# Kernel tuning notes

Measured on AMD Instinct MI355X. Metric: run time of the kernel, lower is better.

## Reference

```python
import jax, jax.numpy as jnp
import numpy as np

DIM = 768
HEADS = 12
HD = DIM // HEADS
B = 8
N = 1025  # 1 cls token + 32x32 patch grid
NUM_CLS = 1
ROPE_BASE = 100.0


def setup_inputs() -> dict:
    key = jax.random.key(0)
    ks = jax.random.split(key, 4)
    x = jax.random.normal(ks[0], (B, N, DIM), jnp.float32)
    xpos = jax.random.randint(ks[1], (B, N, 2), 0, 32)  # int 2D grid coords
    mask_for_attention = jnp.ones((B, N, N), dtype=bool)
    w_qkv = jax.random.normal(ks[2], (3 * DIM, DIM), jnp.float32) / np.sqrt(DIM)
    w_proj = jax.random.normal(ks[3], (DIM, DIM), jnp.float32) / np.sqrt(DIM)
    b_proj = jnp.zeros((DIM,), jnp.float32)
    return {"num_cls": NUM_CLS, "x": x, "xpos": xpos,
            "mask_for_attention": mask_for_attention,
            "w_qkv": w_qkv, "w_proj": w_proj, "b_proj": b_proj}


def _rope1d(t, pos):
    # t: [B,H,N,d], pos: [B,N] float. croco-style: cos/sin table of size d = cat(f,f),
    # rotate_half(x) = cat(-x2, x1).
    d = t.shape[-1]
    inv = 1.0 / (ROPE_BASE ** (jnp.arange(0, d, 2, dtype=jnp.float32) / d))  # [d/2]
    ang = pos[..., None] * inv  # [B,N,d/2]
    cos = jnp.concatenate([jnp.cos(ang), jnp.cos(ang)], -1)[:, None]  # [B,1,N,d]
    sin = jnp.concatenate([jnp.sin(ang), jnp.sin(ang)], -1)[:, None]
    t1, t2 = jnp.split(t, 2, -1)
    rot = jnp.concatenate([-t2, t1], -1)
    return t * cos + rot * sin


def _rope2d(t, pos):
    # first half of head_dim rotated by y coord, second half by x coord
    d = t.shape[-1] // 2
    py = pos[..., 0].astype(t.dtype)
    px = pos[..., 1].astype(t.dtype)
    return jnp.concatenate([_rope1d(t[..., :d], py), _rope1d(t[..., d:], px)], -1)


def reference(num_cls, x, xpos, mask_for_attention, w_qkv, w_proj, b_proj):
    Bb, Nn, C = x.shape
    H, hd = HEADS, C // HEADS
    scale = hd ** -0.5
    # qkv projection -> [B,H,3,N,hd] (mirrors torch .transpose(1,3))
    qkv = (x @ w_qkv.T).reshape(Bb, Nn, 3, H, hd).transpose(0, 3, 2, 1, 4)
    q, k, v = qkv[:, :, 0], qkv[:, :, 1], qkv[:, :, 2]
    # RoPE on non-cls tokens only
    q_nc = _rope2d(q[:, :, num_cls:], xpos[:, num_cls:])
    k_nc = _rope2d(k[:, :, num_cls:], xpos[:, num_cls:])
    # block-structured sim matrix
    sim_rope = jnp.einsum('bhqd,bhkd->bhqk', q_nc, k_nc)            # [B,H,N-c,N-c]
    sim_qcls_k = jnp.einsum('bhqd,bhkd->bhqk', q[:, :, :num_cls], k[:, :, num_cls:])  # [B,H,c,N-c]
    sim_q = jnp.einsum('bhqd,bhkd->bhqk', q, k[:, :, :num_cls])      # [B,H,N,c]
    sim = jnp.concatenate([sim_q,
                           jnp.concatenate([sim_qcls_k, sim_rope], axis=-2)],
                          axis=-1)  # [B,H,N,N]
    sim = sim * scale
    sim = jnp.where(mask_for_attention[:, None], sim, -jnp.inf)
    attn = jax.nn.softmax(sim, axis=-1)
    out = jnp.einsum('bhqk,bhkd->bhqd', attn, v)
    out = out.transpose(0, 2, 1, 3).reshape(Bb, Nn, C)
    return out @ w_proj.T + b_proj
```

## Files before the change

### kernel.cpp

```cpp
#include <hip/hip_runtime.h>

#define Bb 8
#define Nn 1025
#define Hh 12
#define HD 64
#define DIMC 768
#define QKVC 2304
#define MROWS (Bb * Nn)
#define MPADA 8320
#define NPAD 1152
#define K1 0.180336880111f
#define PADCNT 127.0f

typedef _Float16 f16x8 __attribute__((ext_vector_type(8)));
typedef _Float16 f16x4 __attribute__((ext_vector_type(4)));
typedef float f32x4 __attribute__((ext_vector_type(4)));

typedef const __attribute__((address_space(1))) void gv_t;
typedef __attribute__((address_space(3))) void lv_t;

__global__ void cvt3_kernel(const float* __restrict__ s0, _Float16* __restrict__ d0, int n0,
                            const float* __restrict__ s1, _Float16* __restrict__ d1, int n1,
                            const float* __restrict__ s2, _Float16* __restrict__ d2, int n2) {
    int i = blockIdx.x * 256 + threadIdx.x;
    const float* s; _Float16* d; int j;
    if (i < n0)           { s = s0; d = d0; j = i; }
    else if (i < n0 + n1) { s = s1; d = d1; j = i - n0; }
    else if (i < n0 + n1 + n2) { s = s2; d = d2; j = i - n0 - n1; }
    else return;
    float4 v = ((const float4*)s)[j];
    f16x4 h;
    h.x = (_Float16)v.x; h.y = (_Float16)v.y; h.z = (_Float16)v.z; h.w = (_Float16)v.w;
    ((f16x4*)d)[j] = h;
}

template <int MODE>
__global__ void __launch_bounds__(256) gemm_kernel(
    const _Float16* __restrict__ A, const _Float16* __restrict__ W,
    int M, int Ncols, int K,
    _Float16* __restrict__ outh, const float* __restrict__ bias, float* __restrict__ outf)
{
    __shared__ _Float16 As[128 * 32];
    __shared__ _Float16 Ws[128 * 32];
    const int tid = threadIdx.x;
    const int wid = tid >> 6, lane = tid & 63;
    const int quad = lane >> 4, l16 = lane & 15;
    const int bm = blockIdx.x * 128, bn = blockIdx.y * 128;
    const int wm = (wid >> 1) * 64, wn = (wid & 1) * 64;

    f32x4 acc[4][4] = {};

    for (int kk = 0; kk < K; kk += 32) {
#pragma unroll
        for (int c = 0; c < 2; ++c) {
            int s = c * 256 + tid;
            int row = s >> 2, gr = s & 3;
            const _Float16* ga = A + (size_t)(bm + row) * K + kk + gr * 8;
            const _Float16* gw = W + (size_t)(bn + row) * K + kk + gr * 8;
            _Float16* la = As + (size_t)(c * 256 + wid * 64) * 8;
            _Float16* lw = Ws + (size_t)(c * 256 + wid * 64) * 8;
            __builtin_amdgcn_global_load_lds((gv_t*)ga, (lv_t*)la, 16, 0, 0);
            __builtin_amdgcn_global_load_lds((gv_t*)gw, (lv_t*)lw, 16, 0, 0);
        }
        __syncthreads();

        f16x8 af[4], bf[4];
#pragma unroll
        for (int t = 0; t < 4; ++t) {
            af[t] = *(const f16x8*)(As + (size_t)(wm + t * 16 + l16) * 32 + quad * 8);
            bf[t] = *(const f16x8*)(Ws + (size_t)(wn + t * 16 + l16) * 32 + quad * 8);
        }
#pragma unroll
        for (int tm = 0; tm < 4; ++tm)
#pragma unroll
            for (int tn = 0; tn < 4; ++tn)
                acc[tm][tn] = __builtin_amdgcn_mfma_f32_16x16x32_f16(af[tm], bf[tn], acc[tm][tn], 0, 0, 0);
        __syncthreads();
    }

#pragma unroll
    for (int tm = 0; tm < 4; ++tm) {
#pragma unroll
        for (int r = 0; r < 4; ++r) {
            int row = bm + wm + tm * 16 + quad * 4 + r;
            if (row >= M) continue;
#pragma unroll
            for (int tn = 0; tn < 4; ++tn) {
                int col = bn + wn + tn * 16 + l16;
                float val = acc[tm][tn][r];
                if (MODE == 0) {
                    outh[(size_t)row * Ncols + col] = (_Float16)val;
                } else {
                    outf[(size_t)row * Ncols + col] = val + bias[col];
                }
            }
        }
    }
}

__global__ void __launch_bounds__(256) vtrans_kernel(
    const _Float16* __restrict__ qkv, _Float16* __restrict__ vt)
{
    __shared__ _Float16 Ts[64][72];
    const int nt = blockIdx.x;
    const int bh = blockIdx.y;
    const int b = bh / Hh, h = bh - b * Hh;
    const int n0 = nt * 64;
    const int tid = threadIdx.x;
    const _Float16* vsrc = qkv + (size_t)b * Nn * QKVC + 2 * DIMC + h * HD;
#pragma unroll
    for (int i = 0; i < 2; ++i) {
        int t = tid + i * 256;
        int r = t >> 3, cg = t & 7;
        int gn = n0 + r;
        f16x8 v8 = {};
        if (gn < Nn) v8 = *(const f16x8*)(vsrc + (size_t)gn * QKVC + cg * 8);
        *(f16x8*)&Ts[r][cg * 8] = v8;
    }
    __syncthreads();
#pragma unroll
    for (int i = 0; i < 2; ++i) {
        int t = tid + i * 256;
        int d = t >> 3, ng = t & 7;
        f16x8 o;
#pragma unroll
        for (int s = 0; s < 8; ++s) o[s] = Ts[ng * 8 + s][d];
        *(f16x8*)(vt + ((size_t)bh * HD + d) * NPAD + n0 + ng * 8) = o;
    }
}

__global__ void __launch_bounds__(256) rope_kernel(
    _Float16* __restrict__ qkv, const int* __restrict__ xpos,
    float* __restrict__ col0, float* __restrict__ row0)
{
    int gw = blockIdx.x * 4 + (threadIdx.x >> 6);
    int lane = threadIdx.x & 63;
    if (gw >= Bb * Hh * Nn) return;
    int n = gw % Nn;
    int bh = gw / Nn;
    int b = bh / Hh, h = bh - b * Hh;

    _Float16* qp = qkv + ((size_t)b * Nn + n) * QKVC + h * HD;
    _Float16* kp = qp + DIMC;
    const _Float16* qp0 = qkv + (size_t)b * Nn * QKVC + h * HD;
    const _Float16* kp0 = qp0 + DIMC;

    float q = (float)qp[lane];
    float k = (float)kp[lane];
    float q0 = (float)qp0[lane];
    float k0 = (float)kp0[lane];

    float dcol = q * k0, drow = q0 * k;
#pragma unroll
    for (int off = 1; off < 64; off <<= 1) {
        dcol += __shfl_xor(dcol, off);
        drow += __shfl_xor(drow, off);
    }
    if (lane == 0) {
        col0[gw] = dcol * K1;
        row0[gw] = drow * K1;
    }

    if (n >= 1) {
        int py = xpos[((size_t)b * Nn + n) * 2 + 0];
        int px = xpos[((size_t)b * Nn + n) * 2 + 1];
        float pos = (lane < 32) ? (float)py : (float)px;
        int j = lane & 15;
        float inv = __expf(-0.28782313662f * (float)j);
        float ang = pos * inv;
        float sv = __sinf(ang), cv = __cosf(ang);
        float qp_ = __shfl_xor(q, 16);
        float kp_ = __shfl_xor(k, 16);
        float sgn = (lane & 16) ? 1.0f : -1.0f;
        qp[lane] = (_Float16)((q * cv + sgn * qp_ * sv) * K1);
        kp[lane] = (_Float16)(k * cv + sgn * kp_ * sv);
    }
}

__global__ void __launch_bounds__(256) flash_kernel(
    const _Float16* __restrict__ qkv, const _Float16* __restrict__ vt,
    const float* __restrict__ col0, const float* __restrict__ row0,
    _Float16* __restrict__ att)
{
    __shared__ _Float16 Ks[128][72];
    __shared__ _Float16 Vt[64][136];
    __shared__ _Float16 Ps[64][136];

    const int qt = blockIdx.x, bh = blockIdx.y;
    const int b = bh / Hh, h = bh - b * Hh;
    const int tid = threadIdx.x, wid = tid >> 6, lane = tid & 63;
    const int quad = lane >> 4, l16 = lane & 15;
    const int q0row = qt * 64;
    const int c0base = bh * Nn;
    const _Float16* qg = qkv + (size_t)b * Nn * QKVC + h * HD;
    const _Float16* kg = qg + DIMC;
    const _Float16* vtg = vt + (size_t)bh * HD * NPAD;

    const int kR = tid >> 3, kC = (tid & 7) * 8;
    const int vD = tid >> 4, vC = (tid & 15) * 8;

#pragma unroll
    for (int i = 0; i < 2; ++i) {
        int t = tid + i * 256;
        int r = t >> 3, cg = t & 7;
        int gr = q0row + r;
        f16x8 v8 = {};
        if (gr < Nn) v8 = *(const f16x8*)(qg + (size_t)gr * QKVC + cg * 8);
        *(f16x8*)&Ks[r][cg * 8] = v8;
    }
    __syncthreads();
    f16x8 aq[2];
#pragma unroll
    for (int ks = 0; ks < 2; ++ks)
        aq[ks] = *(const f16x8*)&Ks[wid * 16 + l16][ks * 32 + quad * 8];
    __syncthreads();

    f32x4 oacc[4] = {};
    float lrow[4] = {0.f, 0.f, 0.f, 0.f};
    const int gibase = q0row + wid * 16 + quad * 4;

    f16x8 kreg[4], vreg[4];
#pragma unroll
    for (int i = 0; i < 4; ++i) {
        int gr = kR + i * 32;
        f16x8 v8 = {};
        if (gr < Nn) v8 = *(const f16x8*)(kg + (size_t)gr * QKVC + kC);
        kreg[i] = v8;
        vreg[i] = *(const f16x8*)(vtg + (size_t)(vD + i * 16) * NPAD + vC);
    }

    for (int c0 = 0; c0 < Nn; c0 += 128) {
#pragma unroll
        for (int i = 0; i < 4; ++i) {
            *(f16x8*)&Ks[kR + i * 32][kC] = kreg[i];
            *(f16x8*)&Vt[vD + i * 16][vC] = vreg[i];
        }
        __syncthreads();

        int cn = c0 + 128;
        if (cn < Nn) {
#pragma unroll
            for (int i = 0; i < 4; ++i) {
                int gr = cn + kR + i * 32;
                f16x8 v8 = {};
                if (gr < Nn) v8 = *(const f16x8*)(kg + (size_t)gr * QKVC + kC);
                kreg[i] = v8;
                vreg[i] = *(const f16x8*)(vtg + (size_t)(vD + i * 16) * NPAD + cn + vC);
            }
        }

        f32x4 sacc[8] = {};
#pragma unroll
        for (int ks = 0; ks < 2; ++ks)
#pragma unroll
            for (int ct = 0; ct < 8; ++ct) {
                f16x8 bk = *(const f16x8*)&Ks[ct * 16 + l16][ks * 32 + quad * 8];
                sacc[ct] = __builtin_amdgcn_mfma_f32_16x16x32_f16(aq[ks], bk, sacc[ct], 0, 0, 0);
            }

        if (c0 == 0 && l16 == 0) {
#pragma unroll
            for (int r = 0; r < 4; ++r) {
                int gi = gibase + r;
                sacc[0][r] = col0[c0base + (gi < Nn ? gi : 0)];
            }
        }
        if (q0row == 0 && wid == 0 && quad == 0) {
#pragma unroll
            for (int ct = 0; ct < 8; ++ct) {
                int gj = c0 + ct * 16 + l16;
                if (gj < Nn) sacc[ct][0] = row0[c0base + gj];
            }
        }

#pragma unroll
        for (int ct = 0; ct < 8; ++ct) {
#pragma unroll
            for (int r = 0; r < 4; ++r) {
                float p = exp2f(sacc[ct][r]);
                lrow[r] += p;
                Ps[wid * 16 + quad * 4 + r][ct * 16 + l16] = (_Float16)p;
            }
        }

#pragma unroll
        for (int ks = 0; ks < 4; ++ks) {
            f16x8 ap = *(const f16x8*)&Ps[wid * 16 + l16][ks * 32 + quad * 8];
#pragma unroll
            for (int ct = 0; ct < 4; ++ct) {
                f16x8 bv = *(const f16x8*)&Vt[ct * 16 + l16][ks * 32 + quad * 8];
                oacc[ct] = __builtin_amdgcn_mfma_f32_16x16x32_f16(ap, bv, oacc[ct], 0, 0, 0);
            }
        }
        __syncthreads();
    }

#pragma unroll
    for (int r = 0; r < 4; ++r) {
        float l = lrow[r];
#pragma unroll
        for (int off = 1; off < 16; off <<= 1) l += __shfl_xor(l, off);
        l -= PADCNT;
        int gi = q0row + wid * 16 + quad * 4 + r;
        if (gi >= Nn) continue;
        float inv_l = 1.0f / l;
#pragma unroll
        for (int ct = 0; ct < 4; ++ct) {
            att[((size_t)b * Nn + gi) * DIMC + h * HD + ct * 16 + l16] =
                (_Float16)(oacc[ct][r] * inv_l);
        }
    }
}

extern "C" void kernel_launch(void* const* d_in, const int* in_sizes, int n_in,
                              void* d_out, int out_size, void* d_ws, size_t ws_size,
                              hipStream_t stream) {
    const float* x      = (const float*)d_in[1];
    const int*   xpos   = (const int*)d_in[2];
    const float* w_qkv  = (const float*)d_in[4];
    const float* w_proj = (const float*)d_in[5];
    const float* b_proj = (const float*)d_in[6];
    float* out = (float*)d_out;

    char* ws = (char*)d_ws;
    size_t off = 0;
    auto alloc = [&](size_t bytes) {
        char* p = ws + off;
        off += (bytes + 255) & ~(size_t)255;
        return p;
    };
    _Float16* xh     = (_Float16*)alloc((size_t)MPADA * DIMC * 2);
    _Float16* qkvh   = (_Float16*)alloc((size_t)MROWS * QKVC * 2);
    _Float16* vt     = (_Float16*)alloc((size_t)Bb * Hh * HD * NPAD * 2);
    _Float16* wqkvh  = (_Float16*)alloc((size_t)3 * DIMC * DIMC * 2);
    _Float16* wprojh = (_Float16*)alloc((size_t)DIMC * DIMC * 2);
    float* col0      = (float*)alloc((size_t)Bb * Hh * Nn * 4);
    float* row0      = (float*)alloc((size_t)Bb * Hh * Nn * 4);
    _Float16* atth   = xh;

    {
        int n0 = (MROWS * DIMC) / 4;
        int n1 = (3 * DIMC * DIMC) / 4;
        int n2 = (DIMC * DIMC) / 4;
        int nt = n0 + n1 + n2;
        cvt3_kernel<<<(nt + 255) / 256, 256, 0, stream>>>(
            x, xh, n0, w_qkv, wqkvh, n1, w_proj, wprojh, n2);
    }

    gemm_kernel<0><<<dim3(MPADA / 128, QKVC / 128), 256, 0, stream>>>(
        xh, wqkvh, MROWS, QKVC, DIMC, qkvh, nullptr, nullptr);

    rope_kernel<<<(Bb * Hh * Nn) / 4, 256, 0, stream>>>(qkvh, xpos, col0, row0);

    vtrans_kernel<<<dim3(NPAD / 64, Bb * Hh), 256, 0, stream>>>(qkvh, vt);

    flash_kernel<<<dim3((Nn + 63) / 64, Bb * Hh), 256, 0, stream>>>(
        qkvh, vt, col0, row0, atth);

    gemm_kernel<1><<<dim3(MPADA / 128, DIMC / 128), 256, 0, stream>>>(
        atth, wprojh, MROWS, DIMC, DIMC, nullptr, b_proj, out);
}
```

Measured before the change: 303.1 us.

## Keep softmax probabilities in registers via transposed MFMA; double K-step in GEMM

The flash kernel now computes S transposed (K as the A operand, Q as B), so each lane holds a query column. The probabilities are packed to fp16 with cvt_pkrtz and rearranged with cross-lane shuffles into the B operand of the PV MFMA, which removes the LDS round trip through the Ps buffer. It also changes the row-sum reduction and makes the output stores vectorized. Separately, the GEMM loads two 32-wide K slices per barrier pair, which halves the synchronisation count at the cost of double the shared memory. The cvt_pkrtz conversion rounds toward zero, a slight precision change.

```diff
diff --git a/kernel.cpp b/kernel.cpp
--- a/kernel.cpp
+++ b/kernel.cpp
@@ -14,7 +14,9 @@
 
 typedef _Float16 f16x8 __attribute__((ext_vector_type(8)));
 typedef _Float16 f16x4 __attribute__((ext_vector_type(4)));
+typedef _Float16 f16x2 __attribute__((ext_vector_type(2)));
 typedef float f32x4 __attribute__((ext_vector_type(4)));
+typedef int i32x4 __attribute__((ext_vector_type(4)));
 
 typedef const __attribute__((address_space(1))) void gv_t;
 typedef __attribute__((address_space(3))) void lv_t;
@@ -40,8 +42,8 @@
     int M, int Ncols, int K,
     _Float16* __restrict__ outh, const float* __restrict__ bias, float* __restrict__ outf)
 {
-    __shared__ _Float16 As[128 * 32];
-    __shared__ _Float16 Ws[128 * 32];
+    __shared__ _Float16 As[2][128 * 32];
+    __shared__ _Float16 Ws[2][128 * 32];
     const int tid = threadIdx.x;
     const int wid = tid >> 6, lane = tid & 63;
     const int quad = lane >> 4, l16 = lane & 15;
@@ -50,31 +52,37 @@
 
     f32x4 acc[4][4] = {};
 
-    for (int kk = 0; kk < K; kk += 32) {
-#pragma unroll
-        for (int c = 0; c < 2; ++c) {
-            int s = c * 256 + tid;
-            int row = s >> 2, gr = s & 3;
-            const _Float16* ga = A + (size_t)(bm + row) * K + kk + gr * 8;
-            const _Float16* gw = W + (size_t)(bn + row) * K + kk + gr * 8;
-            _Float16* la = As + (size_t)(c * 256 + wid * 64) * 8;
-            _Float16* lw = Ws + (size_t)(c * 256 + wid * 64) * 8;
-            __builtin_amdgcn_global_load_lds((gv_t*)ga, (lv_t*)la, 16, 0, 0);
-            __builtin_amdgcn_global_load_lds((gv_t*)gw, (lv_t*)lw, 16, 0, 0);
+    for (int kk = 0; kk < K; kk += 64) {
+#pragma unroll
+        for (int half = 0; half < 2; ++half) {
+#pragma unroll
+            for (int c = 0; c < 2; ++c) {
+                int s = c * 256 + tid;
+                int row = s >> 2, gr = s & 3;
+                const _Float16* ga = A + (size_t)(bm + row) * K + kk + half * 32 + gr * 8;
+                const _Float16* gw = W + (size_t)(bn + row) * K + kk + half * 32 + gr * 8;
+                _Float16* la = As[half] + (size_t)(c * 256 + wid * 64) * 8;
+                _Float16* lw = Ws[half] + (size_t)(c * 256 + wid * 64) * 8;
+                __builtin_amdgcn_global_load_lds((gv_t*)ga, (lv_t*)la, 16, 0, 0);
+                __builtin_amdgcn_global_load_lds((gv_t*)gw, (lv_t*)lw, 16, 0, 0);
+            }
         }
         __syncthreads();
 
-        f16x8 af[4], bf[4];
-#pragma unroll
-        for (int t = 0; t < 4; ++t) {
-            af[t] = *(const f16x8*)(As + (size_t)(wm + t * 16 + l16) * 32 + quad * 8);
-            bf[t] = *(const f16x8*)(Ws + (size_t)(wn + t * 16 + l16) * 32 + quad * 8);
-        }
-#pragma unroll
-        for (int tm = 0; tm < 4; ++tm)
-#pragma unroll
-            for (int tn = 0; tn < 4; ++tn)
-                acc[tm][tn] = __builtin_amdgcn_mfma_f32_16x16x32_f16(af[tm], bf[tn], acc[tm][tn], 0, 0, 0);
+#pragma unroll
+        for (int half = 0; half < 2; ++half) {
+            f16x8 af[4], bf[4];
+#pragma unroll
+            for (int t = 0; t < 4; ++t) {
+                af[t] = *(const f16x8*)(As[half] + (size_t)(wm + t * 16 + l16) * 32 + quad * 8);
+                bf[t] = *(const f16x8*)(Ws[half] + (size_t)(wn + t * 16 + l16) * 32 + quad * 8);
+            }
+#pragma unroll
+            for (int tm = 0; tm < 4; ++tm)
+#pragma unroll
+                for (int tn = 0; tn < 4; ++tn)
+                    acc[tm][tn] = __builtin_amdgcn_mfma_f32_16x16x32_f16(af[tm], bf[tn], acc[tm][tn], 0, 0, 0);
+        }
         __syncthreads();
     }
 
@@ -184,7 +192,6 @@
 {
     __shared__ _Float16 Ks[128][72];
     __shared__ _Float16 Vt[64][136];
-    __shared__ _Float16 Ps[64][136];
 
     const int qt = blockIdx.x, bh = blockIdx.y;
     const int b = bh / Hh, h = bh - b * Hh;
@@ -215,9 +222,13 @@
         aq[ks] = *(const f16x8*)&Ks[wid * 16 + l16][ks * 32 + quad * 8];
     __syncthreads();
 
-    f32x4 oacc[4] = {};
-    float lrow[4] = {0.f, 0.f, 0.f, 0.f};
-    const int gibase = q0row + wid * 16 + quad * 4;
+    f32x4 oaccT[4] = {};
+    float lrow = 0.f;
+    const int gi = q0row + wid * 16 + l16;
+
+    const int src0 = (((2 * quad) & 3) << 4) + l16;
+    const int src1 = (((2 * quad + 1) & 3) << 4) + l16;
+    const bool hi = (quad >= 2);
 
     f16x8 kreg[4], vreg[4];
 #pragma unroll
@@ -254,60 +265,68 @@
         for (int ks = 0; ks < 2; ++ks)
 #pragma unroll
             for (int ct = 0; ct < 8; ++ct) {
-                f16x8 bk = *(const f16x8*)&Ks[ct * 16 + l16][ks * 32 + quad * 8];
-                sacc[ct] = __builtin_amdgcn_mfma_f32_16x16x32_f16(aq[ks], bk, sacc[ct], 0, 0, 0);
-            }
-
-        if (c0 == 0 && l16 == 0) {
-#pragma unroll
-            for (int r = 0; r < 4; ++r) {
-                int gi = gibase + r;
-                sacc[0][r] = col0[c0base + (gi < Nn ? gi : 0)];
-            }
-        }
-        if (q0row == 0 && wid == 0 && quad == 0) {
-#pragma unroll
-            for (int ct = 0; ct < 8; ++ct) {
-                int gj = c0 + ct * 16 + l16;
-                if (gj < Nn) sacc[ct][0] = row0[c0base + gj];
-            }
-        }
-
+                f16x8 ak = *(const f16x8*)&Ks[ct * 16 + l16][ks * 32 + quad * 8];
+                sacc[ct] = __builtin_amdgcn_mfma_f32_16x16x32_f16(ak, aq[ks], sacc[ct], 0, 0, 0);
+            }
+
+        if (c0 == 0 && quad == 0)
+            sacc[0][0] = col0[c0base + (gi < Nn ? gi : 0)];
+        if (q0row == 0 && wid == 0 && l16 == 0) {
+#pragma unroll
+            for (int ct = 0; ct < 8; ++ct)
+#pragma unroll
+                for (int r = 0; r < 4; ++r) {
+                    int gj = c0 + ct * 16 + quad * 4 + r;
+                    if (gj < Nn) sacc[ct][r] = row0[c0base + gj];
+                }
+        }
+
+        int pkl[8], pkh[8];
 #pragma unroll
         for (int ct = 0; ct < 8; ++ct) {
-#pragma unroll
-            for (int r = 0; r < 4; ++r) {
-                float p = exp2f(sacc[ct][r]);
-                lrow[r] += p;
-                Ps[wid * 16 + quad * 4 + r][ct * 16 + l16] = (_Float16)p;
-            }
+            float p0 = exp2f(sacc[ct][0]);
+            float p1 = exp2f(sacc[ct][1]);
+            float p2 = exp2f(sacc[ct][2]);
+            float p3 = exp2f(sacc[ct][3]);
+            lrow += (p0 + p1) + (p2 + p3);
+            pkl[ct] = __builtin_bit_cast(int, __builtin_amdgcn_cvt_pkrtz(p0, p1));
+            pkh[ct] = __builtin_bit_cast(int, __builtin_amdgcn_cvt_pkrtz(p2, p3));
         }
 
 #pragma unroll
         for (int ks = 0; ks < 4; ++ks) {
-            f16x8 ap = *(const f16x8*)&Ps[wid * 16 + l16][ks * 32 + quad * 8];
+            int a0 = __shfl(pkl[2 * ks], src0), b0 = __shfl(pkl[2 * ks + 1], src0);
+            int a1 = __shfl(pkh[2 * ks], src0), b1 = __shfl(pkh[2 * ks + 1], src0);
+            int a2 = __shfl(pkl[2 * ks], src1), b2 = __shfl(pkl[2 * ks + 1], src1);
+            int a3 = __shfl(pkh[2 * ks], src1), b3 = __shfl(pkh[2 * ks + 1], src1);
+            i32x4 wi;
+            wi.x = hi ? b0 : a0;
+            wi.y = hi ? b1 : a1;
+            wi.z = hi ? b2 : a2;
+            wi.w = hi ? b3 : a3;
+            f16x8 bp = __builtin_bit_cast(f16x8, wi);
 #pragma unroll
             for (int ct = 0; ct < 4; ++ct) {
-                f16x8 bv = *(const f16x8*)&Vt[ct * 16 + l16][ks * 32 + quad * 8];
-                oacc[ct] = __builtin_amdgcn_mfma_f32_16x16x32_f16(ap, bv, oacc[ct], 0, 0, 0);
+                f16x8 av = *(const f16x8*)&Vt[ct * 16 + l16][ks * 32 + quad * 8];
+                oaccT[ct] = __builtin_amdgcn_mfma_f32_16x16x32_f16(av, bp, oaccT[ct], 0, 0, 0);
             }
         }
         __syncthreads();
     }
 
-#pragma unroll
-    for (int r = 0; r < 4; ++r) {
-        float l = lrow[r];
-#pragma unroll
-        for (int off = 1; off < 16; off <<= 1) l += __shfl_xor(l, off);
-        l -= PADCNT;
-        int gi = q0row + wid * 16 + quad * 4 + r;
-        if (gi >= Nn) continue;
+    float l = lrow;
+    l += __shfl_xor(l, 16);
+    l += __shfl_xor(l, 32);
+    l -= PADCNT;
+    if (gi < Nn) {
         float inv_l = 1.0f / l;
+        _Float16* dst = att + ((size_t)b * Nn + gi) * DIMC + h * HD;
 #pragma unroll
         for (int ct = 0; ct < 4; ++ct) {
-            att[((size_t)b * Nn + gi) * DIMC + h * HD + ct * 16 + l16] =
-                (_Float16)(oacc[ct][r] * inv_l);
+            f16x4 o4;
+#pragma unroll
+            for (int r = 0; r < 4; ++r) o4[r] = (_Float16)(oaccT[ct][r] * inv_l);
+            *(f16x4*)(dst + ct * 16 + quad * 4) = o4;
         }
     }
 }
```

Result: slower. 309.2 us (+2.0%).
